# Optimization experiments

Measured on AMD Instinct MI355X. Metric: run time of the kernel, lower is better.

## Reference

```python
import jax, jax.numpy as jnp
import numpy as np

DIM = 1024
HEADS = 8
DIM_HEAD = 64
INNER = HEADS * DIM_HEAD  # 512
B, N = 4, 2048            # batch, text length
T, M = 8, 64              # num media, tokens per media
EPS = 1e-5


def setup_inputs() -> dict:
    key = jax.random.key(0)
    ks = jax.random.split(key, 8)
    x = jax.random.normal(ks[0], (B, N, DIM), dtype=jnp.float32)
    media = jax.random.normal(ks[1], (B, T, M, DIM), dtype=jnp.float32)
    # t evenly spaced media markers in the text stream -> text_time ramps 0..T
    loc = jnp.zeros((B, N), dtype=bool).at[:, jnp.arange(T) * (N // T)].set(True)
    aug_exist_idx = jax.random.randint(ks[2], (B, T), 0, 2, dtype=jnp.int32)
    ln_gamma = jnp.ones((DIM,), dtype=jnp.float32)
    ln_beta = jnp.zeros((DIM,), dtype=jnp.float32)
    Wq = jax.random.normal(ks[3], (DIM, INNER), dtype=jnp.float32) * 0.02
    Wkv = jax.random.normal(ks[4], (DIM, 2 * INNER), dtype=jnp.float32) * 0.02
    Wo = jax.random.normal(ks[5], (INNER, DIM), dtype=jnp.float32) * 0.02
    return {"x": x, "media": media, "media_locations": loc,
            "aug_exist_idx": aug_exist_idx, "ln_gamma": ln_gamma,
            "ln_beta": ln_beta, "Wq": Wq, "Wkv": Wkv, "Wo": Wo}


def reference(x, media, media_locations, aug_exist_idx, ln_gamma, ln_beta, Wq, Wkv, Wo):
    b, t, m, d = media.shape
    n = x.shape[1]
    scale = DIM_HEAD ** -0.5

    # LayerNorm over last dim
    mu = jnp.mean(x, axis=-1, keepdims=True)
    var = jnp.mean(jnp.square(x - mu), axis=-1, keepdims=True)
    xn = (x - mu) * jax.lax.rsqrt(var + EPS) * ln_gamma + ln_beta

    q = xn @ Wq                                   # [b, n, inner]
    kv = media.reshape(b, t * m, d) @ Wkv         # [b, tm, 2*inner]
    k, v = jnp.split(kv, 2, axis=-1)

    def to_heads(z):
        return z.reshape(b, -1, HEADS, DIM_HEAD).transpose(0, 2, 1, 3)
    q, k, v = to_heads(q) * scale, to_heads(k), to_heads(v)

    sim = jnp.einsum('bhid,bhjd->bhij', q, k)     # [b, h, n, tm]
    neg = -jnp.finfo(sim.dtype).max

    # location mask: text token attends only to its immediately preceding media
    text_time = jnp.cumsum(media_locations.astype(jnp.int32), axis=-1)  # [b, n]
    media_time = jnp.repeat(jnp.arange(t, dtype=jnp.int32) + 1, m)      # [tm]
    loc_mask = text_time[:, None, :, None] == media_time[None, None, None, :]
    sim = jnp.where(loc_mask, sim, neg)

    # existence mask: only attend to media whose aug_exist_idx == 1
    exist = jnp.repeat(aug_exist_idx, m, axis=-1)                       # [b, tm]
    exist_mask = (exist == 1)[:, None, None, :]
    sim = jnp.where(exist_mask, sim, neg)

    sim = sim - jax.lax.stop_gradient(jnp.max(sim, axis=-1, keepdims=True))
    attn = jax.nn.softmax(sim, axis=-1)
    # note: original's attn.masked_fill(...) is out-of-place with discarded result -> no-op

    out = jnp.einsum('bhij,bhjd->bhid', attn, v)  # [b, h, n, dh]
    out = out.transpose(0, 2, 1, 3).reshape(b, n, INNER)
    return out @ Wo
```

## Files before the change

### kernel.cpp

```cpp
#include <hip/hip_runtime.h>

typedef unsigned short u16;
typedef __bf16 bf16x8 __attribute__((ext_vector_type(8)));
typedef float f32x4 __attribute__((ext_vector_type(4)));

#define NEGMAX (-3.402823466e38f)

__device__ __forceinline__ u16 f2b(float f) {
  unsigned u = __float_as_uint(f);
  u = u + 0x7fffu + ((u >> 16) & 1u);
  return (u16)(u >> 16);
}
__device__ __forceinline__ float b2f(u16 h) {
  return __uint_as_float(((unsigned)h) << 16);
}

__device__ __forceinline__ void gload16(const void* g, void* l) {
  __builtin_amdgcn_global_load_lds((__attribute__((address_space(1))) void*)g,
                                   (__attribute__((address_space(3))) void*)l, 16, 0, 0);
}

struct PrepSmem {
  union {
    float tile[32][33];
    struct { int sloc[2048]; int tsum[256]; } cs;
  };
};

__device__ __forceinline__ void do_ln(const float* __restrict__ x, const float* __restrict__ g,
                                      const float* __restrict__ be, u16* __restrict__ xn, int blk) {
  const int wave = threadIdx.x >> 6, lane = threadIdx.x & 63;
  const int row = blk * 4 + wave;
  const float4* xr = (const float4*)(x + (size_t)row * 1024);
  float4 v[4];
  float s = 0.f, s2 = 0.f;
#pragma unroll
  for (int j = 0; j < 4; j++) {
    v[j] = xr[j * 64 + lane];
    s += v[j].x + v[j].y + v[j].z + v[j].w;
    s2 += v[j].x * v[j].x + v[j].y * v[j].y + v[j].z * v[j].z + v[j].w * v[j].w;
  }
#pragma unroll
  for (int off = 32; off; off >>= 1) { s += __shfl_xor(s, off); s2 += __shfl_xor(s2, off); }
  const float mu = s * (1.f / 1024.f);
  const float rs = rsqrtf(s2 * (1.f / 1024.f) - mu * mu + 1e-5f);
  ushort4* xo = (ushort4*)(xn + (size_t)row * 1024);
#pragma unroll
  for (int j = 0; j < 4; j++) {
    const float4 gg = ((const float4*)g)[j * 64 + lane];
    const float4 bb = ((const float4*)be)[j * 64 + lane];
    ushort4 o;
    o.x = f2b((v[j].x - mu) * rs * gg.x + bb.x);
    o.y = f2b((v[j].y - mu) * rs * gg.y + bb.y);
    o.z = f2b((v[j].z - mu) * rs * gg.z + bb.z);
    o.w = f2b((v[j].w - mu) * rs * gg.w + bb.w);
    xo[j * 64 + lane] = o;
  }
}

__device__ __forceinline__ void do_transpose(PrepSmem* sm, const float* __restrict__ W,
                                             u16* __restrict__ WT, int K, int N, int bid, int nbx) {
  const int nb = (bid % nbx) * 32, kb = (bid / nbx) * 32;
  const int tx = threadIdx.x & 31, ty = threadIdx.x >> 5;
#pragma unroll
  for (int i = 0; i < 32; i += 8) sm->tile[ty + i][tx] = W[(size_t)(kb + ty + i) * N + nb + tx];
  __syncthreads();
#pragma unroll
  for (int i = 0; i < 32; i += 8) WT[(size_t)(nb + ty + i) * K + kb + tx] = f2b(sm->tile[tx][ty + i]);
}

__device__ __forceinline__ void do_cast(const float* __restrict__ in, u16* __restrict__ out, int blk) {
#pragma unroll
  for (int j = 0; j < 4; j++) {
    const int idx = blk * 1024 + j * 256 + threadIdx.x;
    const float4 v = ((const float4*)in)[idx];
    ushort4 o;
    o.x = f2b(v.x); o.y = f2b(v.y); o.z = f2b(v.z); o.w = f2b(v.w);
    ((ushort4*)out)[idx] = o;
  }
}

__device__ __forceinline__ void do_cumsum(PrepSmem* sm, const int* __restrict__ loc,
                                          int* __restrict__ tt, int b) {
  const int tid = threadIdx.x;
  for (int i = tid; i < 2048; i += 256) sm->cs.sloc[i] = loc[b * 2048 + i];
  __syncthreads();
  int l8[8]; int s = 0;
#pragma unroll
  for (int i = 0; i < 8; i++) { l8[i] = sm->cs.sloc[tid * 8 + i]; s += l8[i]; }
  sm->cs.tsum[tid] = s;
  __syncthreads();
  for (int off = 1; off < 256; off <<= 1) {
    int v = (tid >= off) ? sm->cs.tsum[tid - off] : 0;
    __syncthreads();
    sm->cs.tsum[tid] += v;
    __syncthreads();
  }
  int r = sm->cs.tsum[tid] - s;
#pragma unroll
  for (int i = 0; i < 8; i++) { r += l8[i]; tt[b * 2048 + tid * 8 + i] = r; }
}

__global__ __launch_bounds__(256) void prep_kernel(const float* __restrict__ x,
                                                   const float* __restrict__ gamma,
                                                   const float* __restrict__ beta,
                                                   const float* __restrict__ media,
                                                   const int* __restrict__ loc,
                                                   const float* __restrict__ Wq,
                                                   const float* __restrict__ Wkv,
                                                   const float* __restrict__ Wo,
                                                   u16* __restrict__ xn,
                                                   u16* __restrict__ media_b,
                                                   u16* __restrict__ WqT,
                                                   u16* __restrict__ WkvT,
                                                   u16* __restrict__ WoT,
                                                   int* __restrict__ tt) {
  __shared__ PrepSmem sm;
  int bid = blockIdx.x;
  if (bid < 2048) { do_ln(x, gamma, beta, xn, bid); return; }
  bid -= 2048;
  if (bid < 512) { do_transpose(&sm, Wq, WqT, 1024, 512, bid, 16); return; }
  bid -= 512;
  if (bid < 1024) { do_transpose(&sm, Wkv, WkvT, 1024, 1024, bid, 32); return; }
  bid -= 1024;
  if (bid < 512) { do_transpose(&sm, Wo, WoT, 512, 1024, bid, 32); return; }
  bid -= 512;
  if (bid < 512) { do_cast(media, media_b, bid); return; }
  bid -= 512;
  do_cumsum(&sm, loc, tt, bid);
}

__device__ __forceinline__ void store_c(float* p, float v) { *p = v; }
__device__ __forceinline__ void store_c(u16* p, float v) { *p = f2b(v); }

template <typename OutT>
__device__ __forceinline__ void gemm_body(const u16* __restrict__ A, const u16* __restrict__ BT,
                                          OutT* __restrict__ C, int N, int K, float alpha,
                                          int row0, int col0, u16* lAs, u16* lBs) {
  const int tid = threadIdx.x;
  const int wave = tid >> 6;
  const int lane = tid & 63;
  const int lr = lane & 15, lq = lane >> 4;
  const int wm = (wave >> 1) * 64, wn = (wave & 1) * 64;

  const int trow = tid >> 2;
  const int tcol = (tid & 3) * 8;
  const u16* ga = A + (size_t)(row0 + trow) * K + tcol;
  const u16* gb = BT + (size_t)(col0 + trow) * K + tcol;
  char* lA0 = (char*)lAs + wave * 1024;
  char* lB0 = (char*)lBs + wave * 1024;

  f32x4 acc[4][4] = {};

  for (int k0 = 0; k0 < K; k0 += 32) {
    gload16(ga + k0, lA0);
    gload16(ga + k0 + (size_t)64 * K, lA0 + 4096);
    gload16(gb + k0, lB0);
    gload16(gb + k0 + (size_t)64 * K, lB0 + 4096);
    __syncthreads();
    bf16x8 af[4], bg[4];
#pragma unroll
    for (int mt = 0; mt < 4; mt++)
      af[mt] = *(const bf16x8*)&lAs[(wm + mt * 16 + lr) * 32 + lq * 8];
#pragma unroll
    for (int nt = 0; nt < 4; nt++)
      bg[nt] = *(const bf16x8*)&lBs[(wn + nt * 16 + lr) * 32 + lq * 8];
#pragma unroll
    for (int mt = 0; mt < 4; mt++)
#pragma unroll
      for (int nt = 0; nt < 4; nt++)
        acc[mt][nt] = __builtin_amdgcn_mfma_f32_16x16x32_bf16(af[mt], bg[nt], acc[mt][nt], 0, 0, 0);
    __syncthreads();
  }

#pragma unroll
  for (int mt = 0; mt < 4; mt++) {
#pragma unroll
    for (int nt = 0; nt < 4; nt++) {
      const int r = row0 + wm + mt * 16 + lq * 4;
      const int cc = col0 + wn + nt * 16 + lr;
#pragma unroll
      for (int i = 0; i < 4; i++) {
        store_c(&C[(size_t)(r + i) * N + cc], acc[mt][nt][i] * alpha);
      }
    }
  }
}

__global__ __launch_bounds__(256) void gemm_qkv(const u16* __restrict__ xn,
                                                const u16* __restrict__ WqT,
                                                const u16* __restrict__ mediab,
                                                const u16* __restrict__ WkvT,
                                                u16* __restrict__ qb,
                                                u16* __restrict__ kvb) {
  __shared__ __align__(16) u16 lAs[128 * 32];
  __shared__ __align__(16) u16 lBs[128 * 32];
  int bid = blockIdx.x;
  if (bid < 256) {
    gemm_body<u16>(xn, WqT, qb, 512, 1024, 0.125f, (bid & 63) * 128, (bid >> 6) * 128, lAs, lBs);
  } else {
    bid -= 256;
    gemm_body<u16>(mediab, WkvT, kvb, 1024, 1024, 1.0f, (bid & 15) * 128, (bid >> 4) * 128, lAs, lBs);
  }
}

__global__ __launch_bounds__(256) void gemm_out(const u16* __restrict__ A,
                                                const u16* __restrict__ BT,
                                                float* __restrict__ C) {
  __shared__ __align__(16) u16 lAs[128 * 32];
  __shared__ __align__(16) u16 lBs[128 * 32];
  gemm_body<float>(A, BT, C, 1024, 512, 1.0f, (int)(blockIdx.x & 63) * 128,
                   (int)(blockIdx.x >> 6) * 128, lAs, lBs);
}

__global__ __launch_bounds__(256) void vt_kernel(const u16* __restrict__ kv, u16* __restrict__ vt) {
  __shared__ u16 tile[32][34];
  const int b = blockIdx.z;
  const int kb = blockIdx.x * 32;
  const int db = blockIdx.y * 32;
  const int tx = threadIdx.x & 31, ty = threadIdx.x >> 5;
#pragma unroll
  for (int i = 0; i < 32; i += 8)
    tile[ty + i][tx] = kv[((size_t)(b * 512 + kb + ty + i)) * 1024 + 512 + db + tx];
  __syncthreads();
#pragma unroll
  for (int i = 0; i < 32; i += 8)
    vt[((size_t)(b * 512 + db + ty + i)) * 512 + kb + tx] = tile[tx][ty + i];
}

__global__ __launch_bounds__(256) void fattn_kernel(const u16* __restrict__ qb,
                                                    const u16* __restrict__ kv,
                                                    const u16* __restrict__ vt,
                                                    const int* __restrict__ tt,
                                                    const int* __restrict__ aug,
                                                    u16* __restrict__ out) {
  const int bh = blockIdx.x;
  const int b = bh >> 3, h = bh & 7;
  const int q0 = blockIdx.y * 64;
  const int tid = threadIdx.x;
  const int wave = tid >> 6, lane = tid & 63;
  const int lr = lane & 15, lq = lane >> 4;

  __shared__ __align__(16) u16 lQ[64 * 72];
  __shared__ __align__(16) u16 lK[64 * 72];
  __shared__ __align__(16) u16 lVT[64 * 72];
  __shared__ __align__(16) u16 lP[4][16 * 72];
  __shared__ int stt[64];
  __shared__ int sex[8];

  const int srow = tid >> 2, seg = tid & 3;

  {
    const uint4* src = (const uint4*)(qb + ((size_t)(b * 2048 + q0 + srow)) * 512 + h * 64 + seg * 16);
    uint4 a0 = src[0], a1 = src[1];
    *(uint4*)&lQ[srow * 72 + seg * 16] = a0;
    *(uint4*)&lQ[srow * 72 + seg * 16 + 8] = a1;
  }
  if (tid < 64) stt[tid] = tt[b * 2048 + q0 + tid];
  if (tid < 8) sex[tid] = aug[b * 8 + tid];
  __syncthreads();

  bf16x8 af[2];
#pragma unroll
  for (int ks = 0; ks < 2; ks++)
    af[ks] = *(const bf16x8*)&lQ[(wave * 16 + lr) * 72 + ks * 32 + lq * 8];

  float m_run[4], l_run[4];
  f32x4 o[4] = {};
#pragma unroll
  for (int i = 0; i < 4; i++) { m_run[i] = NEGMAX; l_run[i] = 0.f; }

  u16* lPw = lP[wave];

  for (int kt = 0; kt < 8; kt++) {
    const uint4* ksrc = (const uint4*)(kv + ((size_t)(b * 512 + kt * 64 + srow)) * 1024 + h * 64 + seg * 16);
    uint4 k0 = ksrc[0], k1 = ksrc[1];
    const uint4* vsrc = (const uint4*)(vt + ((size_t)(b * 512 + h * 64 + srow)) * 512 + kt * 64 + seg * 16);
    uint4 v0 = vsrc[0], v1 = vsrc[1];
    __syncthreads();
    *(uint4*)&lK[srow * 72 + seg * 16] = k0;
    *(uint4*)&lK[srow * 72 + seg * 16 + 8] = k1;
    *(uint4*)&lVT[srow * 72 + seg * 16] = v0;
    *(uint4*)&lVT[srow * 72 + seg * 16 + 8] = v1;
    __syncthreads();

    bf16x8 kf[4][2];
#pragma unroll
    for (int nt = 0; nt < 4; nt++)
#pragma unroll
      for (int ks = 0; ks < 2; ks++)
        kf[nt][ks] = *(const bf16x8*)&lK[(nt * 16 + lr) * 72 + ks * 32 + lq * 8];
    f32x4 s[4] = {};
#pragma unroll
    for (int nt = 0; nt < 4; nt++)
#pragma unroll
      for (int ks = 0; ks < 2; ks++)
        s[nt] = __builtin_amdgcn_mfma_f32_16x16x32_bf16(af[ks], kf[nt][ks], s[nt], 0, 0, 0);

    const int ex = sex[kt];
    float mnew[4], alpha[4];
#pragma unroll
    for (int i = 0; i < 4; i++) {
      const int tti = stt[wave * 16 + lq * 4 + i];
      const bool valid = (tti == kt + 1) && (ex == 1);
      float mx = NEGMAX;
#pragma unroll
      for (int nt = 0; nt < 4; nt++) {
        float sv = valid ? s[nt][i] : NEGMAX;
        s[nt][i] = sv;
        mx = fmaxf(mx, sv);
      }
      mx = fmaxf(mx, __shfl_xor(mx, 1));
      mx = fmaxf(mx, __shfl_xor(mx, 2));
      mx = fmaxf(mx, __shfl_xor(mx, 4));
      mx = fmaxf(mx, __shfl_xor(mx, 8));
      mnew[i] = fmaxf(m_run[i], mx);
      alpha[i] = __expf(m_run[i] - mnew[i]);
      m_run[i] = mnew[i];
    }

#pragma unroll
    for (int i = 0; i < 4; i++) {
      float rs = 0.f;
#pragma unroll
      for (int nt = 0; nt < 4; nt++) {
        float pv = __expf(s[nt][i] - mnew[i]);
        u16 pb = f2b(pv);
        lPw[(lq * 4 + i) * 72 + nt * 16 + lr] = pb;
        rs += b2f(pb);
      }
      rs += __shfl_xor(rs, 1);
      rs += __shfl_xor(rs, 2);
      rs += __shfl_xor(rs, 4);
      rs += __shfl_xor(rs, 8);
      l_run[i] = l_run[i] * alpha[i] + rs;
    }
    asm volatile("s_waitcnt lgkmcnt(0)" ::: "memory");

    bf16x8 pa[2], vf[4][2];
#pragma unroll
    for (int ks = 0; ks < 2; ks++)
      pa[ks] = *(const bf16x8*)&lPw[lr * 72 + ks * 32 + lq * 8];
#pragma unroll
    for (int nt = 0; nt < 4; nt++)
#pragma unroll
      for (int ks = 0; ks < 2; ks++)
        vf[nt][ks] = *(const bf16x8*)&lVT[(nt * 16 + lr) * 72 + ks * 32 + lq * 8];
#pragma unroll
    for (int nt = 0; nt < 4; nt++) {
#pragma unroll
      for (int i = 0; i < 4; i++) o[nt][i] *= alpha[i];
#pragma unroll
      for (int ks = 0; ks < 2; ks++)
        o[nt] = __builtin_amdgcn_mfma_f32_16x16x32_bf16(pa[ks], vf[nt][ks], o[nt], 0, 0, 0);
    }
  }

#pragma unroll
  for (int i = 0; i < 4; i++) {
    const float inv = 1.0f / l_run[i];
    const int qrow = q0 + wave * 16 + lq * 4 + i;
#pragma unroll
    for (int nt = 0; nt < 4; nt++) {
      out[((size_t)(b * 2048 + qrow)) * 512 + h * 64 + nt * 16 + lr] = f2b(o[nt][i] * inv);
    }
  }
}

extern "C" void kernel_launch(void* const* d_in, const int* in_sizes, int n_in,
                              void* d_out, int out_size, void* d_ws, size_t ws_size,
                              hipStream_t stream) {
  (void)in_sizes; (void)n_in; (void)out_size; (void)ws_size;
  const float* x     = (const float*)d_in[0];
  const float* media = (const float*)d_in[1];
  const int*   loc   = (const int*)d_in[2];
  const int*   aug   = (const int*)d_in[3];
  const float* gamma = (const float*)d_in[4];
  const float* beta  = (const float*)d_in[5];
  const float* Wq    = (const float*)d_in[6];
  const float* Wkv   = (const float*)d_in[7];
  const float* Wo    = (const float*)d_in[8];
  float* out = (float*)d_out;

  char* p = (char*)d_ws;
  u16*   xn      = (u16*)(p + 0);
  u16*   attnout = (u16*)(p + 0);
  u16*   qb      = (u16*)(p + (16u << 20));
  u16*   kv      = (u16*)(p + (24u << 20));
  u16*   vtb     = (u16*)(p + (28u << 20));
  u16*   media_b = (u16*)(p + (30u << 20));
  u16*   WqT     = (u16*)(p + (34u << 20));
  u16*   WkvT    = (u16*)(p + (35u << 20));
  u16*   WoT     = (u16*)(p + (37u << 20));
  int*   ttime   = (int*)(p + (38u << 20));

  prep_kernel<<<dim3(4612), 256, 0, stream>>>(x, gamma, beta, media, loc, Wq, Wkv, Wo,
                                              xn, media_b, WqT, WkvT, WoT, ttime);
  gemm_qkv<<<dim3(384), 256, 0, stream>>>(xn, WqT, media_b, WkvT, qb, kv);
  vt_kernel<<<dim3(16, 16, 4), 256, 0, stream>>>(kv, vtb);
  fattn_kernel<<<dim3(32, 32), 256, 0, stream>>>(qb, kv, vtb, ttime, aug, attnout);
  gemm_out<<<dim3(512), 256, 0, stream>>>(attnout, WoT, out);
}
```

Baseline: 182.9 us.

## Exploit block-diagonal mask: attend only to own chunk, mean-fill fully masked rows

Precomputes a per-token media chunk index that folds the location mask and the existence mask together. Attention now processes only the chunks a query tile actually needs and uses single-chunk softmax with no running max. Fully masked rows get the mean of V, which the V GEMM accumulates with atomics. Q-projection tiles and output-GEMM tiles whose rows are all masked are skipped, and the output tile is filled with a precomputed mean(V)·Wo row. The V-transpose kernel is removed in favour of strided LDS reads of V, at the cost of atomics and extra branching.

```diff
diff --git a/kernel.cpp b/kernel.cpp
--- a/kernel.cpp
+++ b/kernel.cpp
@@ -81,7 +81,8 @@
 }
 
 __device__ __forceinline__ void do_cumsum(PrepSmem* sm, const int* __restrict__ loc,
-                                          int* __restrict__ tt, int b) {
+                                          const int* __restrict__ aug, int* __restrict__ cch,
+                                          float* __restrict__ meanv, int b) {
   const int tid = threadIdx.x;
   for (int i = tid; i < 2048; i += 256) sm->cs.sloc[i] = loc[b * 2048 + i];
   __syncthreads();
@@ -98,7 +99,14 @@
   }
   int r = sm->cs.tsum[tid] - s;
 #pragma unroll
-  for (int i = 0; i < 8; i++) { r += l8[i]; tt[b * 2048 + tid * 8 + i] = r; }
+  for (int i = 0; i < 8; i++) {
+    r += l8[i];
+    const int tt = r;
+    const bool valid = (tt >= 1 && tt <= 8) && (aug[b * 8 + tt - 1] == 1);
+    cch[b * 2048 + tid * 8 + i] = valid ? tt - 1 : -1;
+  }
+  meanv[b * 512 + tid] = 0.f;
+  meanv[b * 512 + 256 + tid] = 0.f;
 }
 
 __global__ __launch_bounds__(256) void prep_kernel(const float* __restrict__ x,
@@ -106,6 +114,7 @@
                                                    const float* __restrict__ beta,
                                                    const float* __restrict__ media,
                                                    const int* __restrict__ loc,
+                                                   const int* __restrict__ aug,
                                                    const float* __restrict__ Wq,
                                                    const float* __restrict__ Wkv,
                                                    const float* __restrict__ Wo,
@@ -114,7 +123,8 @@
                                                    u16* __restrict__ WqT,
                                                    u16* __restrict__ WkvT,
                                                    u16* __restrict__ WoT,
-                                                   int* __restrict__ tt) {
+                                                   int* __restrict__ cch,
+                                                   float* __restrict__ meanv) {
   __shared__ PrepSmem sm;
   int bid = blockIdx.x;
   if (bid < 2048) { do_ln(x, gamma, beta, xn, bid); return; }
@@ -127,16 +137,17 @@
   bid -= 512;
   if (bid < 512) { do_cast(media, media_b, bid); return; }
   bid -= 512;
-  do_cumsum(&sm, loc, tt, bid);
+  do_cumsum(&sm, loc, aug, cch, meanv, bid);
 }
 
 __device__ __forceinline__ void store_c(float* p, float v) { *p = v; }
 __device__ __forceinline__ void store_c(u16* p, float v) { *p = f2b(v); }
 
-template <typename OutT>
+template <typename OutT, bool MV>
 __device__ __forceinline__ void gemm_body(const u16* __restrict__ A, const u16* __restrict__ BT,
                                           OutT* __restrict__ C, int N, int K, float alpha,
-                                          int row0, int col0, u16* lAs, u16* lBs) {
+                                          int row0, int col0, u16* lAs, u16* lBs,
+                                          float* __restrict__ meanv) {
   const int tid = threadIdx.x;
   const int wave = tid >> 6;
   const int lane = tid & 63;
@@ -185,6 +196,23 @@
       }
     }
   }
+
+  if constexpr (MV) {
+    if (col0 >= 512) {
+      const int bmv = row0 >> 9;
+#pragma unroll
+      for (int nt = 0; nt < 4; nt++) {
+        float ps = 0.f;
+#pragma unroll
+        for (int mt = 0; mt < 4; mt++)
+#pragma unroll
+          for (int i = 0; i < 4; i++) ps += acc[mt][nt][i];
+        ps += __shfl_xor(ps, 16);
+        ps += __shfl_xor(ps, 32);
+        if (lq == 0) atomicAdd(&meanv[bmv * 512 + (col0 - 512) + wn + nt * 16 + lr], ps);
+      }
+    }
+  }
 }
 
 __global__ __launch_bounds__(256) void gemm_qkv(const u16* __restrict__ xn,
@@ -192,72 +220,127 @@
                                                 const u16* __restrict__ mediab,
                                                 const u16* __restrict__ WkvT,
                                                 u16* __restrict__ qb,
-                                                u16* __restrict__ kvb) {
+                                                u16* __restrict__ kvb,
+                                                const int* __restrict__ cch,
+                                                float* __restrict__ meanv) {
   __shared__ __align__(16) u16 lAs[128 * 32];
   __shared__ __align__(16) u16 lBs[128 * 32];
+  __shared__ int sflag;
   int bid = blockIdx.x;
   if (bid < 256) {
-    gemm_body<u16>(xn, WqT, qb, 512, 1024, 0.125f, (bid & 63) * 128, (bid >> 6) * 128, lAs, lBs);
+    const int row0 = (bid & 63) * 128, col0 = (bid >> 6) * 128;
+    if (threadIdx.x == 0) sflag = 0;
+    __syncthreads();
+    if (threadIdx.x < 128 && cch[row0 + threadIdx.x] >= 0) sflag = 1;
+    __syncthreads();
+    if (!sflag) return;
+    gemm_body<u16, false>(xn, WqT, qb, 512, 1024, 0.125f, row0, col0, lAs, lBs, nullptr);
   } else {
     bid -= 256;
-    gemm_body<u16>(mediab, WkvT, kvb, 1024, 1024, 1.0f, (bid & 15) * 128, (bid >> 4) * 128, lAs, lBs);
+    gemm_body<u16, true>(mediab, WkvT, kvb, 1024, 1024, 1.0f, (bid & 15) * 128, (bid >> 4) * 128,
+                         lAs, lBs, meanv);
   }
 }
 
 __global__ __launch_bounds__(256) void gemm_out(const u16* __restrict__ A,
                                                 const u16* __restrict__ BT,
-                                                float* __restrict__ C) {
+                                                float* __restrict__ C,
+                                                const int* __restrict__ cch,
+                                                const float* __restrict__ fbrow) {
   __shared__ __align__(16) u16 lAs[128 * 32];
   __shared__ __align__(16) u16 lBs[128 * 32];
-  gemm_body<float>(A, BT, C, 1024, 512, 1.0f, (int)(blockIdx.x & 63) * 128,
-                   (int)(blockIdx.x >> 6) * 128, lAs, lBs);
-}
-
-__global__ __launch_bounds__(256) void vt_kernel(const u16* __restrict__ kv, u16* __restrict__ vt) {
-  __shared__ u16 tile[32][34];
-  const int b = blockIdx.z;
-  const int kb = blockIdx.x * 32;
-  const int db = blockIdx.y * 32;
-  const int tx = threadIdx.x & 31, ty = threadIdx.x >> 5;
-#pragma unroll
-  for (int i = 0; i < 32; i += 8)
-    tile[ty + i][tx] = kv[((size_t)(b * 512 + kb + ty + i)) * 1024 + 512 + db + tx];
-  __syncthreads();
-#pragma unroll
-  for (int i = 0; i < 32; i += 8)
-    vt[((size_t)(b * 512 + db + ty + i)) * 512 + kb + tx] = tile[tx][ty + i];
+  __shared__ int sflag;
+  const int bid = blockIdx.x;
+  const int row0 = (bid & 63) * 128, col0 = (bid >> 6) * 128;
+  if (threadIdx.x == 0) sflag = 0;
+  __syncthreads();
+  if (threadIdx.x < 128 && cch[row0 + threadIdx.x] >= 0) sflag = 1;
+  __syncthreads();
+  if (!sflag) {
+    const int b = row0 >> 11;
+    const float4 fv = *(const float4*)(fbrow + b * 1024 + col0 + (threadIdx.x & 31) * 4);
+    for (int r = threadIdx.x >> 5; r < 128; r += 8)
+      *(float4*)(C + (size_t)(row0 + r) * 1024 + col0 + (threadIdx.x & 31) * 4) = fv;
+    return;
+  }
+  gemm_body<float, false>(A, BT, C, 1024, 512, 1.0f, row0, col0, lAs, lBs, nullptr);
 }
 
 __global__ __launch_bounds__(256) void fattn_kernel(const u16* __restrict__ qb,
                                                     const u16* __restrict__ kv,
-                                                    const u16* __restrict__ vt,
-                                                    const int* __restrict__ tt,
-                                                    const int* __restrict__ aug,
-                                                    u16* __restrict__ out) {
-  const int bh = blockIdx.x;
-  const int b = bh >> 3, h = bh & 7;
-  const int q0 = blockIdx.y * 64;
+                                                    const int* __restrict__ cch,
+                                                    const float* __restrict__ meanv,
+                                                    const u16* __restrict__ WoT,
+                                                    u16* __restrict__ out,
+                                                    float* __restrict__ fbrow) {
+  const int bid = blockIdx.x;
   const int tid = threadIdx.x;
+
+  if (bid >= 1024) {
+    __shared__ float smv[512];
+    const int blk = bid - 1024;
+    const int b = blk >> 2, n0 = (blk & 3) * 256;
+    smv[tid] = meanv[b * 512 + tid] * (1.f / 512.f);
+    smv[tid + 256] = meanv[b * 512 + 256 + tid] * (1.f / 512.f);
+    __syncthreads();
+    const int n = n0 + tid;
+    const u16* wr = WoT + (size_t)n * 512;
+    float acc = 0.f;
+#pragma unroll 4
+    for (int k = 0; k < 512; k += 8) {
+      const uint4 w = *(const uint4*)(wr + k);
+      acc += smv[k + 0] * __uint_as_float(w.x << 16);
+      acc += smv[k + 1] * __uint_as_float(w.x & 0xffff0000u);
+      acc += smv[k + 2] * __uint_as_float(w.y << 16);
+      acc += smv[k + 3] * __uint_as_float(w.y & 0xffff0000u);
+      acc += smv[k + 4] * __uint_as_float(w.z << 16);
+      acc += smv[k + 5] * __uint_as_float(w.z & 0xffff0000u);
+      acc += smv[k + 6] * __uint_as_float(w.w << 16);
+      acc += smv[k + 7] * __uint_as_float(w.w & 0xffff0000u);
+    }
+    fbrow[b * 1024 + n] = acc;
+    return;
+  }
+
+  const int b = bid >> 8, h = (bid >> 5) & 7;
+  const int q0 = (bid & 31) * 64;
   const int wave = tid >> 6, lane = tid & 63;
   const int lr = lane & 15, lq = lane >> 4;
 
   __shared__ __align__(16) u16 lQ[64 * 72];
   __shared__ __align__(16) u16 lK[64 * 72];
-  __shared__ __align__(16) u16 lVT[64 * 72];
+  __shared__ __align__(16) u16 lV[64 * 72];
   __shared__ __align__(16) u16 lP[4][16 * 72];
-  __shared__ int stt[64];
-  __shared__ int sex[8];
+  __shared__ int scch[64];
+  __shared__ int smask;
+
+  if (tid == 0) smask = 0;
+  __syncthreads();
+  if (tid < 64) {
+    const int v = cch[b * 2048 + q0 + tid];
+    scch[tid] = v;
+    if (v >= 0) atomicOr(&smask, 1 << v);
+  }
+  __syncthreads();
+  const int mask = smask;
+
+  if (mask == 0) {
+    const int c = tid & 63;
+    const u16 mb = f2b(meanv[b * 512 + h * 64 + c] * (1.f / 512.f));
+    for (int r = tid >> 6; r < 64; r += 4)
+      out[((size_t)(b * 2048 + q0 + r)) * 512 + h * 64 + c] = mb;
+    return;
+  }
 
   const int srow = tid >> 2, seg = tid & 3;
-
   {
     const uint4* src = (const uint4*)(qb + ((size_t)(b * 2048 + q0 + srow)) * 512 + h * 64 + seg * 16);
-    uint4 a0 = src[0], a1 = src[1];
-    *(uint4*)&lQ[srow * 72 + seg * 16] = a0;
-    *(uint4*)&lQ[srow * 72 + seg * 16 + 8] = a1;
-  }
-  if (tid < 64) stt[tid] = tt[b * 2048 + q0 + tid];
-  if (tid < 8) sex[tid] = aug[b * 8 + tid];
+    *(uint4*)&lQ[srow * 72 + seg * 16] = src[0];
+    *(uint4*)&lQ[srow * 72 + seg * 16 + 8] = src[1];
+  }
+  int rc[4];
+#pragma unroll
+  for (int i = 0; i < 4; i++) rc[i] = scch[wave * 16 + lq * 4 + i];
   __syncthreads();
 
   bf16x8 af[2];
@@ -265,23 +348,21 @@
   for (int ks = 0; ks < 2; ks++)
     af[ks] = *(const bf16x8*)&lQ[(wave * 16 + lr) * 72 + ks * 32 + lq * 8];
 
-  float m_run[4], l_run[4];
+  float l_run[4] = {0.f, 0.f, 0.f, 0.f};
   f32x4 o[4] = {};
-#pragma unroll
-  for (int i = 0; i < 4; i++) { m_run[i] = NEGMAX; l_run[i] = 0.f; }
-
   u16* lPw = lP[wave];
 
-  for (int kt = 0; kt < 8; kt++) {
-    const uint4* ksrc = (const uint4*)(kv + ((size_t)(b * 512 + kt * 64 + srow)) * 1024 + h * 64 + seg * 16);
+  for (int c = 0; c < 8; c++) {
+    if (!((mask >> c) & 1)) continue;
+    const uint4* ksrc = (const uint4*)(kv + ((size_t)(b * 512 + c * 64 + srow)) * 1024 + h * 64 + seg * 16);
     uint4 k0 = ksrc[0], k1 = ksrc[1];
-    const uint4* vsrc = (const uint4*)(vt + ((size_t)(b * 512 + h * 64 + srow)) * 512 + kt * 64 + seg * 16);
+    const uint4* vsrc = (const uint4*)(kv + ((size_t)(b * 512 + c * 64 + srow)) * 1024 + 512 + h * 64 + seg * 16);
     uint4 v0 = vsrc[0], v1 = vsrc[1];
     __syncthreads();
     *(uint4*)&lK[srow * 72 + seg * 16] = k0;
     *(uint4*)&lK[srow * 72 + seg * 16 + 8] = k1;
-    *(uint4*)&lVT[srow * 72 + seg * 16] = v0;
-    *(uint4*)&lVT[srow * 72 + seg * 16 + 8] = v1;
+    *(uint4*)&lV[srow * 72 + seg * 16] = v0;
+    *(uint4*)&lV[srow * 72 + seg * 16 + 8] = v1;
     __syncthreads();
 
     bf16x8 kf[4][2];
@@ -297,35 +378,21 @@
       for (int ks = 0; ks < 2; ks++)
         s[nt] = __builtin_amdgcn_mfma_f32_16x16x32_bf16(af[ks], kf[nt][ks], s[nt], 0, 0, 0);
 
-    const int ex = sex[kt];
-    float mnew[4], alpha[4];
 #pragma unroll
     for (int i = 0; i < 4; i++) {
-      const int tti = stt[wave * 16 + lq * 4 + i];
-      const bool valid = (tti == kt + 1) && (ex == 1);
+      const bool match = (rc[i] == c);
       float mx = NEGMAX;
 #pragma unroll
-      for (int nt = 0; nt < 4; nt++) {
-        float sv = valid ? s[nt][i] : NEGMAX;
-        s[nt][i] = sv;
-        mx = fmaxf(mx, sv);
-      }
+      for (int nt = 0; nt < 4; nt++) mx = fmaxf(mx, s[nt][i]);
       mx = fmaxf(mx, __shfl_xor(mx, 1));
       mx = fmaxf(mx, __shfl_xor(mx, 2));
       mx = fmaxf(mx, __shfl_xor(mx, 4));
       mx = fmaxf(mx, __shfl_xor(mx, 8));
-      mnew[i] = fmaxf(m_run[i], mx);
-      alpha[i] = __expf(m_run[i] - mnew[i]);
-      m_run[i] = mnew[i];
-    }
-
-#pragma unroll
-    for (int i = 0; i < 4; i++) {
       float rs = 0.f;
 #pragma unroll
       for (int nt = 0; nt < 4; nt++) {
-        float pv = __expf(s[nt][i] - mnew[i]);
-        u16 pb = f2b(pv);
+        const float pv = match ? __expf(s[nt][i] - mx) : 0.f;
+        const u16 pb = f2b(pv);
         lPw[(lq * 4 + i) * 72 + nt * 16 + lr] = pb;
         rs += b2f(pb);
       }
@@ -333,36 +400,40 @@
       rs += __shfl_xor(rs, 2);
       rs += __shfl_xor(rs, 4);
       rs += __shfl_xor(rs, 8);
-      l_run[i] = l_run[i] * alpha[i] + rs;
+      if (match) l_run[i] = rs;
     }
     asm volatile("s_waitcnt lgkmcnt(0)" ::: "memory");
 
-    bf16x8 pa[2], vf[4][2];
+    bf16x8 pa[2];
 #pragma unroll
     for (int ks = 0; ks < 2; ks++)
       pa[ks] = *(const bf16x8*)&lPw[lr * 72 + ks * 32 + lq * 8];
 #pragma unroll
-    for (int nt = 0; nt < 4; nt++)
-#pragma unroll
-      for (int ks = 0; ks < 2; ks++)
-        vf[nt][ks] = *(const bf16x8*)&lVT[(nt * 16 + lr) * 72 + ks * 32 + lq * 8];
-#pragma unroll
     for (int nt = 0; nt < 4; nt++) {
 #pragma unroll
-      for (int i = 0; i < 4; i++) o[nt][i] *= alpha[i];
-#pragma unroll
-      for (int ks = 0; ks < 2; ks++)
-        o[nt] = __builtin_amdgcn_mfma_f32_16x16x32_bf16(pa[ks], vf[nt][ks], o[nt], 0, 0, 0);
+      for (int ks = 0; ks < 2; ks++) {
+        union { bf16x8 v; u16 s[8]; } vf;
+#pragma unroll
+        for (int j = 0; j < 8; j++)
+          vf.s[j] = lV[(ks * 32 + lq * 8 + j) * 72 + nt * 16 + lr];
+        o[nt] = __builtin_amdgcn_mfma_f32_16x16x32_bf16(pa[ks], vf.v, o[nt], 0, 0, 0);
+      }
     }
   }
 
 #pragma unroll
   for (int i = 0; i < 4; i++) {
-    const float inv = 1.0f / l_run[i];
     const int qrow = q0 + wave * 16 + lq * 4 + i;
-#pragma unroll
-    for (int nt = 0; nt < 4; nt++) {
-      out[((size_t)(b * 2048 + qrow)) * 512 + h * 64 + nt * 16 + lr] = f2b(o[nt][i] * inv);
+    if (rc[i] >= 0) {
+      const float inv = 1.0f / l_run[i];
+#pragma unroll
+      for (int nt = 0; nt < 4; nt++)
+        out[((size_t)(b * 2048 + qrow)) * 512 + h * 64 + nt * 16 + lr] = f2b(o[nt][i] * inv);
+    } else {
+#pragma unroll
+      for (int nt = 0; nt < 4; nt++)
+        out[((size_t)(b * 2048 + qrow)) * 512 + h * 64 + nt * 16 + lr] =
+            f2b(meanv[b * 512 + h * 64 + nt * 16 + lr] * (1.f / 512.f));
     }
   }
 }
@@ -387,17 +458,17 @@
   u16*   attnout = (u16*)(p + 0);
   u16*   qb      = (u16*)(p + (16u << 20));
   u16*   kv      = (u16*)(p + (24u << 20));
-  u16*   vtb     = (u16*)(p + (28u << 20));
-  u16*   media_b = (u16*)(p + (30u << 20));
-  u16*   WqT     = (u16*)(p + (34u << 20));
-  u16*   WkvT    = (u16*)(p + (35u << 20));
-  u16*   WoT     = (u16*)(p + (37u << 20));
-  int*   ttime   = (int*)(p + (38u << 20));
-
-  prep_kernel<<<dim3(4612), 256, 0, stream>>>(x, gamma, beta, media, loc, Wq, Wkv, Wo,
-                                              xn, media_b, WqT, WkvT, WoT, ttime);
-  gemm_qkv<<<dim3(384), 256, 0, stream>>>(xn, WqT, media_b, WkvT, qb, kv);
-  vt_kernel<<<dim3(16, 16, 4), 256, 0, stream>>>(kv, vtb);
-  fattn_kernel<<<dim3(32, 32), 256, 0, stream>>>(qb, kv, vtb, ttime, aug, attnout);
-  gemm_out<<<dim3(512), 256, 0, stream>>>(attnout, WoT, out);
-}
+  u16*   media_b = (u16*)(p + (28u << 20));
+  u16*   WqT     = (u16*)(p + (32u << 20));
+  u16*   WkvT    = (u16*)(p + (33u << 20));
+  u16*   WoT     = (u16*)(p + (35u << 20));
+  int*   cch     = (int*)(p + (36u << 20));
+  float* meanv   = (float*)(p + (36u << 20) + (32u << 10));
+  float* fbrow   = (float*)(p + (36u << 20) + (64u << 10));
+
+  prep_kernel<<<dim3(4612), 256, 0, stream>>>(x, gamma, beta, media, loc, aug, Wq, Wkv, Wo,
+                                              xn, media_b, WqT, WkvT, WoT, cch, meanv);
+  gemm_qkv<<<dim3(384), 256, 0, stream>>>(xn, WqT, media_b, WkvT, qb, kv, cch, meanv);
+  fattn_kernel<<<dim3(1040), 256, 0, stream>>>(qb, kv, cch, meanv, WoT, attnout, fbrow);
+  gemm_out<<<dim3(512), 256, 0, stream>>>(attnout, WoT, out, cch, fbrow);
+}
```

New measurement: 159.7 us. -12.7%, faster.
